# Performance work log

Hardware: AMD Instinct MI355X
Metric: run time of the kernel (lower is better)

The kernel has to match this reference:

```python
import jax, jax.numpy as jnp
import numpy as np

K = 16  # memory_topk

def signed_abs_softmax(x, axis=-1):
    # sign(x) * softmax(|x|): the module's 'signed_abs_softmax' route/edge compression
    return jnp.sign(x) * jax.nn.softmax(jnp.abs(x), axis=axis)

def unit_norm(v, eps=1e-6):
    return v / (jnp.linalg.norm(v, axis=-1, keepdims=True) + eps)

def setup_inputs() -> dict:
    key = jax.random.key(0)
    ks = jax.random.split(key, 7)
    B, T, D, S, R = 8, 2048, 512, 2048, 64
    std = 0.02
    return {
        "x": jax.random.normal(ks[0], (B, T, D), jnp.float32),
        "init_state": std * jax.random.normal(ks[1], (S,), jnp.float32),
        "init_val": std * jax.random.normal(ks[2], (S, D), jnp.float32),
        "route_a": std * jax.random.normal(ks[3], (D, R), jnp.float32),
        "route_b": std * jax.random.normal(ks[4], (R, S), jnp.float32),
        "pair_a": std * jax.random.normal(ks[5], (D, R), jnp.float32),
        "pair_b": std * jax.random.normal(ks[6], (D, R), jnp.float32),
    }

def reference(x, init_state, init_val, route_a, route_b, pair_a, pair_b):
    B, T, D = x.shape
    S = init_val.shape[0]
    b_idx = jnp.arange(B)[:, None, None]

    # --- initialize memory level (signed-softmax state, unit-norm values) ---
    state = jnp.broadcast_to(signed_abs_softmax(init_state), (B, S))
    val = jnp.broadcast_to(unit_norm(init_val), (B, S, D))

    # --- SparseTransition write: topk route tokens -> slots, scatter-add ---
    scores = jnp.einsum('btd,dr,rs->bts', x, route_a, route_b)   # [B,T,S] low-rank route
    _, idx = jax.lax.top_k(jnp.abs(scores), K)                    # [B,T,K] topk by magnitude
    g = jnp.take_along_axis(scores, idx, axis=-1)                 # signed gathered scores
    w = signed_abs_softmax(g, axis=-1)                            # route compression
    v = unit_norm(x)                                              # use_direction_only=True
    val_delta = jnp.zeros((B, S, D), x.dtype).at[b_idx, idx].add(w[..., None] * v[:, :, None, :])
    state_delta = jnp.zeros((B, S), x.dtype).at[b_idx, idx].add(jax.nn.softplus(g))
    state = signed_abs_softmax(state + state_delta, axis=-1)      # merge='add' + signed softmax state
    val = unit_norm(val + val_delta)                              # merge='add' + unit-norm values

    # --- SparsePropagation: topk pairwise edges among slots, residual mix ---
    q = jnp.einsum('bsd,dr->bsr', val, pair_a)
    kk = jnp.einsum('bsd,dr->bsr', val, pair_b)
    p = jnp.einsum('bir,bjr->bij', q, kk)                         # [B,S,S] low-rank pairwise
    _, eidx = jax.lax.top_k(jnp.abs(p), K)                        # [B,S,K] topk edges per slot
    pe = jnp.take_along_axis(p, eidx, axis=-1)
    ew = signed_abs_softmax(pe, axis=-1)                          # edge compression
    nbr = val[b_idx, eidx]                                        # [B,S,K,D] gather neighbor values
    delta = jnp.einsum('bsk,bskd->bsd', ew, nbr)
    val = unit_norm(val + delta)                                  # residual + unit-norm

    # pack (state, val) into one array: [B,S,1+D]
    return jnp.concatenate([state[..., None], val], axis=-1)
```

## Files before the change

### kernel.cpp

```cpp
#include <hip/hip_runtime.h>
#include <cmath>

namespace {
constexpr int B = 8;
constexpr int T = 2048;
constexpr int D = 512;
constexpr int S = 2048;
constexpr int R = 64;
constexpr int KTOP = 16;
constexpr int NT = 8;
constexpr int NR = 16;
constexpr int NI = 8;
constexpr int CAP = 256;
constexpr int OVFCAP = 32768;

__device__ __forceinline__ float signf(float v) {
    return (v > 0.f) ? 1.f : ((v < 0.f) ? -1.f : 0.f);
}

__device__ __forceinline__ void topk16_row(float* __restrict__ row,
                                           unsigned long long* __restrict__ cand,
                                           int lane, float& myg, int& myj) {
    const float4* p4 = (const float4*)row;
    float lmax = 0.f;
#pragma unroll
    for (int i = 0; i < 8; i++) {
        float4 v = p4[lane + 64 * i];
        lmax = fmaxf(lmax, fmaxf(fmaxf(fabsf(v.x), fabsf(v.y)),
                                 fmaxf(fabsf(v.z), fabsf(v.w))));
    }
    {
        float v = lmax;
#pragma unroll
        for (int size = 2; size <= 64; size <<= 1) {
#pragma unroll
            for (int stride = size >> 1; stride > 0; stride >>= 1) {
                float o = __shfl_xor(v, stride, 64);
                bool takeMax = ((lane & size) == 0) == ((lane & stride) == 0);
                v = takeMax ? fmaxf(v, o) : fminf(v, o);
            }
        }
        lmax = __shfl(v, 15);
    }
    float t = lmax;
    int cnt = 0;
#pragma unroll
    for (int i = 0; i < 8; i++) {
        float4 v = p4[lane + 64 * i];
        cnt += (fabsf(v.x) >= t) + (fabsf(v.y) >= t) +
               (fabsf(v.z) >= t) + (fabsf(v.w) >= t);
    }
    int off = cnt;
#pragma unroll
    for (int d = 1; d < 64; d <<= 1) {
        int o = __shfl_up(off, d, 64);
        if (lane >= d) off += o;
    }
    int total = __shfl(off, 63);
    int base = off - cnt;

    if (total <= 64) {
        int pos = base;
#pragma unroll
        for (int i = 0; i < 8; i++) {
            float4 v = p4[lane + 64 * i];
            int jb = 4 * (lane + 64 * i);
            float c[4] = {v.x, v.y, v.z, v.w};
#pragma unroll
            for (int cc = 0; cc < 4; cc++) {
                if (fabsf(c[cc]) >= t) {
                    unsigned ab = __float_as_uint(c[cc]) & 0x7fffffffu;
                    cand[pos++] = ((unsigned long long)ab << 11) |
                                  (unsigned)(2047 - (jb + cc));
                }
            }
        }
        unsigned long long key = (lane < total) ? cand[lane] : 0ull;
#pragma unroll
        for (int size = 2; size <= 64; size <<= 1) {
#pragma unroll
            for (int stride = size >> 1; stride > 0; stride >>= 1) {
                unsigned long long o = __shfl_xor((long long)key, stride, 64);
                bool takeMax = ((lane & size) == 0) == ((lane & stride) == 0);
                key = (takeMax == (key > o)) ? key : o;
            }
        }
        myg = 0.f; myj = 0;
        if (lane < KTOP) {
            myj = 2047 - (int)(key & 2047ull);
            myg = row[myj];
        }
    } else {
        myg = 0.f; myj = 0;
        for (int k = 0; k < KTOP; k++) {
            float bv = -1.f, bs = 0.f; int bj = 0;
#pragma unroll
            for (int i = 0; i < 8; i++) {
                float4 v = p4[lane + 64 * i];
                int jb = 4 * (lane + 64 * i);
                { float a = fabsf(v.x); if (a > bv) { bv = a; bs = v.x; bj = jb; } }
                { float a = fabsf(v.y); if (a > bv) { bv = a; bs = v.y; bj = jb + 1; } }
                { float a = fabsf(v.z); if (a > bv) { bv = a; bs = v.z; bj = jb + 2; } }
                { float a = fabsf(v.w); if (a > bv) { bv = a; bs = v.w; bj = jb + 3; } }
            }
#pragma unroll
            for (int off2 = 32; off2 > 0; off2 >>= 1) {
                float ov = __shfl_xor(bv, off2, 64);
                float os = __shfl_xor(bs, off2, 64);
                int   oj = __shfl_xor(bj, off2, 64);
                if (ov > bv || (ov == bv && oj < bj)) { bv = ov; bs = os; bj = oj; }
            }
            if (lane == k) { myg = bs; myj = bj; }
            if (lane == 0) row[bj] = 0.f;
        }
    }
}
}

__global__ void __launch_bounds__(512, 4) k_score(const float* __restrict__ x,
                                                  const float* __restrict__ route_a,
                                                  const float* __restrict__ route_b,
                                                  float* __restrict__ state_ws,
                                                  float* __restrict__ coef,
                                                  int* __restrict__ bincount,
                                                  int* __restrict__ binlist,
                                                  int* __restrict__ ovf_cnt,
                                                  int* __restrict__ ovf_key,
                                                  float* __restrict__ ovf_c) {
    __shared__ __align__(16) char smem[NT * S * 4];
    __shared__ __align__(16) float xr[NT][R];
    __shared__ unsigned long long cand[NT][64];
    float (*sc)[S] = (float(*)[S])smem;
    float (*xs)[D] = (float(*)[D])smem;
    float (*red4)[512] = (float(*)[512])smem;

    int tid = threadIdx.x;
    int lane = tid & 63, wv = tid >> 6;
    int blk = ((blockIdx.x & 7) << 8) | (blockIdx.x >> 3);
    int tb = blk * NT;
    int b = tb >> 11;
    int t0 = tb & (T - 1);

    {
        const float4* xg = (const float4*)(x + (size_t)tb * D);
        float4* xls = (float4*)smem;
        xls[tid] = xg[tid];
        xls[tid + 512] = xg[tid + 512];
    }
    __syncthreads();

    float xinv;
    {
        const float4* xst = (const float4*)&xs[wv][0];
        float4 x0 = xst[lane], x1 = xst[lane + 64];
        float ssx = x0.x * x0.x + x0.y * x0.y + x0.z * x0.z + x0.w * x0.w
                  + x1.x * x1.x + x1.y * x1.y + x1.z * x1.z + x1.w * x1.w;
#pragma unroll
        for (int off = 32; off > 0; off >>= 1) ssx += __shfl_xor(ssx, off, 64);
        xinv = 1.0f / (sqrtf(ssx) + 1e-6f);
    }

    {
        int r = lane;
        float acc[NT];
#pragma unroll
        for (int tt = 0; tt < NT; tt++) acc[tt] = 0.f;
        for (int d0 = wv * 64; d0 < wv * 64 + 64; d0 += 4) {
            float a0 = route_a[(size_t)(d0 + 0) * R + r];
            float a1 = route_a[(size_t)(d0 + 1) * R + r];
            float a2 = route_a[(size_t)(d0 + 2) * R + r];
            float a3 = route_a[(size_t)(d0 + 3) * R + r];
#pragma unroll
            for (int tt = 0; tt < NT; tt++) {
                float4 xv = *(const float4*)&xs[tt][d0];
                acc[tt] += xv.x * a0 + xv.y * a1 + xv.z * a2 + xv.w * a3;
            }
        }
        __syncthreads();
#pragma unroll
        for (int tt = 0; tt < NT; tt++) red4[tt][tid] = acc[tt];
        __syncthreads();
        {
            int tt2 = tid >> 6, r2 = tid & 63;
            float s = 0.f;
#pragma unroll
            for (int g = 0; g < 8; g++) s += red4[tt2][g * 64 + r2];
            xr[tt2][r2] = s;
        }
        __syncthreads();
    }

    {
        const float4* rb4 = (const float4*)route_b;
        int j4 = tid;
        float4 acc[NT];
#pragma unroll
        for (int tt = 0; tt < NT; tt++) acc[tt] = make_float4(0.f, 0.f, 0.f, 0.f);
        for (int r0 = 0; r0 < R; r0 += 4) {
            float4 xv[NT];
#pragma unroll
            for (int tt = 0; tt < NT; tt++) xv[tt] = *(const float4*)&xr[tt][r0];
#define SCORE_STEP(dr, comp)                                                   \
            {                                                                  \
                float4 bv = rb4[(size_t)(r0 + dr) * (S / 4) + j4];             \
                _Pragma("unroll")                                              \
                for (int tt = 0; tt < NT; tt++) {                              \
                    float c = xv[tt].comp;                                     \
                    acc[tt].x += c * bv.x; acc[tt].y += c * bv.y;              \
                    acc[tt].z += c * bv.z; acc[tt].w += c * bv.w;              \
                }                                                              \
            }
            SCORE_STEP(0, x) SCORE_STEP(1, y) SCORE_STEP(2, z) SCORE_STEP(3, w)
#undef SCORE_STEP
        }
#pragma unroll
        for (int tt = 0; tt < NT; tt++)
            ((float4*)&sc[tt][0])[j4] = acc[tt];
    }
    __syncthreads();

    int tt = wv;
    int tloc = t0 + tt;
    int tglob = tb + tt;

    float myg; int myj;
    topk16_row(&sc[tt][0], &cand[wv][0], lane, myg, myj);

    float m = __shfl(fabsf(myg), 0);
    float e = (lane < KTOP) ? expf(fabsf(myg) - m) : 0.f;
    float esum = e;
#pragma unroll
    for (int off = 8; off > 0; off >>= 1) esum += __shfl_xor(esum, off, 64);
    esum = __shfl(esum, 0);
    float w = signf(myg) * e / esum;
    float coefv = w * xinv;

    if (lane < KTOP) {
        float sp = (myg > 20.f) ? myg : log1pf(expf(myg));
        atomicAdd(&state_ws[(size_t)b * S + myj], sp);
        int pos = atomicAdd(&bincount[(size_t)b * S + myj], 1);
        if (pos < CAP) {
            binlist[((size_t)b * S + myj) * CAP + pos] = (tloc << 4) | lane;
            coef[(size_t)tglob * KTOP + lane] = coefv;
        } else {
            int i = atomicAdd(ovf_cnt, 1);
            if (i < OVFCAP) {
                ovf_key[i] = ((b * S + myj) << 11) | tloc;
                ovf_c[i] = coefv;
            }
        }
    }
}

__global__ void __launch_bounds__(256) k_accum(const float* __restrict__ x,
                                               const float* __restrict__ init_val,
                                               const float* __restrict__ coef,
                                               const int* __restrict__ bincount,
                                               const int* __restrict__ binlist,
                                               const int* __restrict__ ovf_cnt,
                                               const int* __restrict__ ovf_key,
                                               const float* __restrict__ ovf_c,
                                               float* __restrict__ val1) {
    int lane = threadIdx.x & 63, wv = threadIdx.x >> 6;
    int blk = ((blockIdx.x & 7) << 9) | (blockIdx.x >> 3);
    int row = blk * 4 + wv;
    int b = row >> 11;
    int s_idx = row & (S - 1);

    const float4* src = (const float4*)(init_val + (size_t)s_idx * D);
    float4 a0 = src[lane], a1 = src[lane + 64];
    {
        float ss0 = a0.x * a0.x + a0.y * a0.y + a0.z * a0.z + a0.w * a0.w
                  + a1.x * a1.x + a1.y * a1.y + a1.z * a1.z + a1.w * a1.w;
#pragma unroll
        for (int off = 32; off > 0; off >>= 1) ss0 += __shfl_xor(ss0, off, 64);
        float bsc = 1.0f / (sqrtf(ss0) + 1e-6f);
        a0.x *= bsc; a0.y *= bsc; a0.z *= bsc; a0.w *= bsc;
        a1.x *= bsc; a1.y *= bsc; a1.z *= bsc; a1.w *= bsc;
    }

    int n = bincount[row]; if (n > CAP) n = CAP;
    const int* lp = binlist + (size_t)row * CAP;
    for (int base = 0; base < n; base += 64) {
        int mm = n - base; if (mm > 64) mm = 64;
        int ent = 0; float cc = 0.f;
        if (lane < mm) {
            ent = lp[base + lane];
            cc = coef[((size_t)b * T + (ent >> 4)) * KTOP + (ent & 15)];
        }
        int e0 = __shfl(ent, 0);
        const float4* xp4 = (const float4*)(x + ((size_t)b * T + (e0 >> 4)) * D);
        float4 v0 = xp4[lane], v1 = xp4[lane + 64];
        for (int k = 0; k < mm; k++) {
            float c = __shfl(cc, k);
            float4 c0 = v0, c1 = v1;
            if (k + 1 < mm) {
                int e2 = __shfl(ent, k + 1);
                const float4* np4 = (const float4*)(x + ((size_t)b * T + (e2 >> 4)) * D);
                v0 = np4[lane]; v1 = np4[lane + 64];
            }
            a0.x += c * c0.x; a0.y += c * c0.y; a0.z += c * c0.z; a0.w += c * c0.w;
            a1.x += c * c1.x; a1.y += c * c1.y; a1.z += c * c1.z; a1.w += c * c1.w;
        }
    }

    int oc = *ovf_cnt; if (oc > OVFCAP) oc = OVFCAP;
    for (int i = 0; i < oc; i++) {
        int key = ovf_key[i];
        if ((key >> 11) == row) {
            float c = ovf_c[i];
            int tg = ((row >> 11) << 11) | (key & 2047);
            const float4* xp4 = (const float4*)(x + (size_t)tg * D);
            float4 v0 = xp4[lane], v1 = xp4[lane + 64];
            a0.x += c * v0.x; a0.y += c * v0.y; a0.z += c * v0.z; a0.w += c * v0.w;
            a1.x += c * v1.x; a1.y += c * v1.y; a1.z += c * v1.z; a1.w += c * v1.w;
        }
    }

    float ss = a0.x * a0.x + a0.y * a0.y + a0.z * a0.z + a0.w * a0.w
             + a1.x * a1.x + a1.y * a1.y + a1.z * a1.z + a1.w * a1.w;
#pragma unroll
    for (int off = 32; off > 0; off >>= 1) ss += __shfl_xor(ss, off, 64);
    float sc = 1.0f / (sqrtf(ss) + 1e-6f);
    a0.x *= sc; a0.y *= sc; a0.z *= sc; a0.w *= sc;
    a1.x *= sc; a1.y *= sc; a1.z *= sc; a1.w *= sc;
    float4* vp4 = (float4*)(val1 + (size_t)row * D);
    vp4[lane] = a0; vp4[lane + 64] = a1;
}

__global__ void __launch_bounds__(512) k_state_red(const float* __restrict__ init_state,
                                                   const float* __restrict__ state_ws,
                                                   float* base_ws,
                                                   float* sm_m, float* sm_inv) {
    __shared__ float red[16];
    __shared__ float base_lds[S];
    int tid = threadIdx.x, lane = tid & 63, wv = tid >> 6;

    float4 v = ((const float4*)init_state)[tid];
    float m = fmaxf(fmaxf(fabsf(v.x), fabsf(v.y)), fmaxf(fabsf(v.z), fabsf(v.w)));
#pragma unroll
    for (int off = 32; off > 0; off >>= 1) m = fmaxf(m, __shfl_xor(m, off, 64));
    if (lane == 0) red[wv] = m;
    __syncthreads();
    float M = red[0];
#pragma unroll
    for (int i = 1; i < 8; i++) M = fmaxf(M, red[i]);
    __syncthreads();
    float s = expf(fabsf(v.x) - M) + expf(fabsf(v.y) - M) +
              expf(fabsf(v.z) - M) + expf(fabsf(v.w) - M);
#pragma unroll
    for (int off = 32; off > 0; off >>= 1) s += __shfl_xor(s, off, 64);
    if (lane == 0) red[wv] = s;
    __syncthreads();
    float SUM = 0.f;
#pragma unroll
    for (int i = 0; i < 8; i++) SUM += red[i];
    float inv = 1.0f / SUM;
    float4 bo;
    bo.x = signf(v.x) * expf(fabsf(v.x) - M) * inv;
    bo.y = signf(v.y) * expf(fabsf(v.y) - M) * inv;
    bo.z = signf(v.z) * expf(fabsf(v.z) - M) * inv;
    bo.w = signf(v.w) * expf(fabsf(v.w) - M) * inv;
    ((float4*)base_ws)[tid] = bo;
    ((float4*)base_lds)[tid] = bo;
    __syncthreads();

    int b = wv;
    const float4* dp = (const float4*)(state_ws + (size_t)b * S);
    const float4* bp = (const float4*)base_lds;
    float4 c[8];
    float vm = 0.f;
#pragma unroll
    for (int i = 0; i < 8; i++) {
        float4 dv = dp[lane + 64 * i];
        float4 bv = bp[lane + 64 * i];
        c[i].x = bv.x + dv.x; c[i].y = bv.y + dv.y;
        c[i].z = bv.z + dv.z; c[i].w = bv.w + dv.w;
        vm = fmaxf(vm, fmaxf(fmaxf(fabsf(c[i].x), fabsf(c[i].y)),
                             fmaxf(fabsf(c[i].z), fabsf(c[i].w))));
    }
#pragma unroll
    for (int off = 32; off > 0; off >>= 1) vm = fmaxf(vm, __shfl_xor(vm, off, 64));
    float sum = 0.f;
#pragma unroll
    for (int i = 0; i < 8; i++) {
        sum += expf(fabsf(c[i].x) - vm) + expf(fabsf(c[i].y) - vm) +
               expf(fabsf(c[i].z) - vm) + expf(fabsf(c[i].w) - vm);
    }
#pragma unroll
    for (int off = 32; off > 0; off >>= 1) sum += __shfl_xor(sum, off, 64);
    if (lane == 0) { sm_m[b] = vm; sm_inv[b] = 1.0f / sum; }
}

__global__ void __launch_bounds__(256) k_qk(const float* __restrict__ val1,
                                            const float* __restrict__ pair_a,
                                            const float* __restrict__ pair_b,
                                            float* __restrict__ q,
                                            float* __restrict__ kkT) {
    __shared__ __align__(16) float vrow[NR][D];
    __shared__ float redq[256];
    __shared__ float redk[256];
    int tid = threadIdx.x;
    int blk = ((blockIdx.x & 7) << 7) | (blockIdx.x >> 3);
    int rowbase = blk * NR;
    int b = rowbase >> 11;
    int sbase = rowbase & (S - 1);
    {
        const float4* gv = (const float4*)(val1 + (size_t)rowbase * D);
        float4* lv = (float4*)&vrow[0][0];
        for (int i = tid; i < NR * D / 4; i += 256) lv[i] = gv[i];
    }
    __syncthreads();
    int r = tid & 63, grp = tid >> 6;
    float accq[NR], acck[NR];
#pragma unroll
    for (int rr = 0; rr < NR; rr++) { accq[rr] = 0.f; acck[rr] = 0.f; }
    for (int d0 = grp * 128; d0 < grp * 128 + 128; d0 += 4) {
#pragma unroll
        for (int dd = 0; dd < 4; dd++) {
            float a  = pair_a[(size_t)(d0 + dd) * R + r];
            float bb = pair_b[(size_t)(d0 + dd) * R + r];
#pragma unroll
            for (int rr = 0; rr < NR; rr++) {
                float v = vrow[rr][d0 + dd];
                accq[rr] += v * a;
                acck[rr] += v * bb;
            }
        }
    }
    for (int rr = 0; rr < NR; rr++) {
        redq[tid] = accq[rr]; redk[tid] = acck[rr];
        __syncthreads();
        if (tid < 64) {
            float qv = redq[tid] + redq[tid + 64] + redq[tid + 128] + redq[tid + 192];
            float kv = redk[tid] + redk[tid + 64] + redk[tid + 128] + redk[tid + 192];
            q[(size_t)(rowbase + rr) * R + tid] = qv;
            kkT[((size_t)b * R + tid) * S + (sbase + rr)] = kv;
        }
        __syncthreads();
    }
}

__global__ void __launch_bounds__(512) k_pscore(const float* __restrict__ q,
                                                const float* __restrict__ kkT,
                                                int* __restrict__ eidx,
                                                float* __restrict__ ew_g) {
    __shared__ __align__(16) float prow[NI][S];
    __shared__ __align__(16) float qrow[NI][R];
    __shared__ unsigned long long cand[NI][64];

    int tid = threadIdx.x;
    int lane = tid & 63, wv = tid >> 6;
    int blk = ((blockIdx.x & 7) << 8) | (blockIdx.x >> 3);
    int ibase = blk * NI;
    int b = ibase >> 11;

    {
        int rr = tid >> 6, r = tid & 63;
        qrow[rr][r] = q[(size_t)(ibase + rr) * R + r];
    }
    __syncthreads();

    {
        const float4* kk4 = (const float4*)(kkT + (size_t)b * R * S);
        int j4 = tid;
        float4 acc[NI];
#pragma unroll
        for (int rr = 0; rr < NI; rr++) acc[rr] = make_float4(0.f, 0.f, 0.f, 0.f);
        for (int r0 = 0; r0 < R; r0 += 4) {
            float4 qv[NI];
#pragma unroll
            for (int rr = 0; rr < NI; rr++) qv[rr] = *(const float4*)&qrow[rr][r0];
#define P_STEP(dr, comp)                                                       \
            {                                                                  \
                float4 kv = kk4[(size_t)(r0 + dr) * (S / 4) + j4];             \
                _Pragma("unroll")                                              \
                for (int rr = 0; rr < NI; rr++) {                              \
                    float c = qv[rr].comp;                                     \
                    acc[rr].x += c * kv.x; acc[rr].y += c * kv.y;              \
                    acc[rr].z += c * kv.z; acc[rr].w += c * kv.w;              \
                }                                                              \
            }
            P_STEP(0, x) P_STEP(1, y) P_STEP(2, z) P_STEP(3, w)
#undef P_STEP
        }
#pragma unroll
        for (int rr = 0; rr < NI; rr++)
            ((float4*)&prow[rr][0])[j4] = acc[rr];
    }
    __syncthreads();

    int row = ibase + wv;
    float myg; int myj;
    topk16_row(&prow[wv][0], &cand[wv][0], lane, myg, myj);

    float m = __shfl(fabsf(myg), 0);
    float e = (lane < KTOP) ? expf(fabsf(myg) - m) : 0.f;
    float esum = e;
#pragma unroll
    for (int off = 8; off > 0; off >>= 1) esum += __shfl_xor(esum, off, 64);
    esum = __shfl(esum, 0);
    float myw = signf(myg) * e / esum;

    if (lane < KTOP) {
        eidx[(size_t)row * KTOP + lane] = myj;
        ew_g[(size_t)row * KTOP + lane] = myw;
    }
}

__global__ void __launch_bounds__(256) k_mix(const int* __restrict__ eidx,
                                             const float* __restrict__ ew_g,
                                             const float* __restrict__ val1,
                                             const float* __restrict__ base_ws,
                                             const float* __restrict__ state_ws,
                                             const float* __restrict__ sm_m,
                                             const float* __restrict__ sm_inv,
                                             float* __restrict__ out) {
    int lane = threadIdx.x & 63, wv = threadIdx.x >> 6;
    int blk = ((blockIdx.x & 7) << 9) | (blockIdx.x >> 3);
    int row = blk * 4 + wv;
    int b = row >> 11;

    int e_i = 0; float e_w = 0.f;
    if (lane < KTOP) {
        e_i = eidx[(size_t)row * KTOP + lane];
        e_w = ew_g[(size_t)row * KTOP + lane];
    }

    const float4* self4 = (const float4*)(val1 + (size_t)row * D);
    float4 a0 = self4[lane], a1 = self4[lane + 64];
#pragma unroll
    for (int k = 0; k < KTOP; k++) {
        int j = __shfl(e_i, k);
        float w = __shfl(e_w, k);
        const float4* nb4 = (const float4*)(val1 + ((size_t)b * S + j) * D);
        float4 v0 = nb4[lane], v1 = nb4[lane + 64];
        a0.x += w * v0.x; a0.y += w * v0.y; a0.z += w * v0.z; a0.w += w * v0.w;
        a1.x += w * v1.x; a1.y += w * v1.y; a1.z += w * v1.z; a1.w += w * v1.w;
    }
    float ss = a0.x * a0.x + a0.y * a0.y + a0.z * a0.z + a0.w * a0.w
             + a1.x * a1.x + a1.y * a1.y + a1.z * a1.z + a1.w * a1.w;
#pragma unroll
    for (int off = 32; off > 0; off >>= 1) ss += __shfl_xor(ss, off, 64);
    float sc = 1.0f / (sqrtf(ss) + 1e-6f);
    float* op = out + (size_t)row * (D + 1) + 1;
    int d0 = 4 * lane;
    op[d0 + 0] = a0.x * sc; op[d0 + 1] = a0.y * sc;
    op[d0 + 2] = a0.z * sc; op[d0 + 3] = a0.w * sc;
    op[256 + d0 + 0] = a1.x * sc; op[256 + d0 + 1] = a1.y * sc;
    op[256 + d0 + 2] = a1.z * sc; op[256 + d0 + 3] = a1.w * sc;

    if (lane == 0) {
        float vv = base_ws[row & (S - 1)] + state_ws[row];
        out[(size_t)row * (D + 1)] =
            signf(vv) * expf(fabsf(vv) - sm_m[b]) * sm_inv[b];
    }
}

extern "C" void kernel_launch(void* const* d_in, const int* in_sizes, int n_in,
                              void* d_out, int out_size, void* d_ws, size_t ws_size,
                              hipStream_t stream) {
    (void)in_sizes; (void)n_in; (void)out_size; (void)ws_size;
    const float* x          = (const float*)d_in[0];
    const float* init_state = (const float*)d_in[1];
    const float* init_val   = (const float*)d_in[2];
    const float* route_a    = (const float*)d_in[3];
    const float* route_b    = (const float*)d_in[4];
    const float* pair_a     = (const float*)d_in[5];
    const float* pair_b     = (const float*)d_in[6];
    float* out = (float*)d_out;

    float* ws       = (float*)d_ws;
    float* val1     = ws;
    float* q        = val1 + (size_t)B * S * D;
    float* kkT      = q    + (size_t)B * S * R;
    float* coef     = kkT  + (size_t)B * R * S;
    int*   binlist  = (int*)(coef + (size_t)B * T * KTOP);
    float* state_ws = (float*)(binlist + (size_t)B * S * CAP);
    int*   bincount = (int*)(state_ws + (size_t)B * S);
    int*   ovf_cnt  = bincount + (size_t)B * S;
    int*   ovf_key  = ovf_cnt + 16;
    float* ovf_c    = (float*)(ovf_key + OVFCAP);
    float* base_ws  = ovf_c + OVFCAP;
    float* sm_m     = base_ws + S;
    float* sm_inv   = sm_m + B;
    int*   eidx     = binlist;
    float* ew       = (float*)(binlist + (size_t)B * S * KTOP);

    hipMemsetAsync(state_ws, 0, (size_t)(2 * B * S + 16) * sizeof(int), stream);
    hipLaunchKernelGGL(k_score, dim3(B * T / NT), dim3(512), 0, stream,
                       x, route_a, route_b, state_ws, coef, bincount, binlist,
                       ovf_cnt, ovf_key, ovf_c);
    hipLaunchKernelGGL(k_state_red, dim3(1), dim3(512), 0, stream,
                       init_state, state_ws, base_ws, sm_m, sm_inv);
    hipLaunchKernelGGL(k_accum, dim3(B * S / 4), dim3(256), 0, stream,
                       x, init_val, coef, bincount, binlist,
                       ovf_cnt, ovf_key, ovf_c, val1);
    hipLaunchKernelGGL(k_qk, dim3(B * S / NR), dim3(256), 0, stream,
                       val1, pair_a, pair_b, q, kkT);
    hipLaunchKernelGGL(k_pscore, dim3(B * S / NI), dim3(512), 0, stream,
                       q, kkT, eidx, ew);
    hipLaunchKernelGGL(k_mix, dim3(B * S / 4), dim3(256), 0, stream,
                       eidx, ew, val1, base_ws, state_ws, sm_m, sm_inv, out);
}
```

Measured before the change: 410.9 us.

## Fuse q/k projection into accumulate kernel and mix into pairwise top-k kernel

The q/k low-rank projection is folded into the value-accumulate kernel, so each block projects its four freshly normalized rows straight from shared memory instead of re-reading val1. The neighbor mix and output write are folded into the pairwise-score top-k kernel, which removes the eidx/ew round trip and two launches. The cost is less reuse of pair_a/pair_b per block (4 rows instead of 16) and a heavier pscore kernel whose occupancy and latency hiding may change.

```diff
diff --git a/kernel.cpp b/kernel.cpp
--- a/kernel.cpp
+++ b/kernel.cpp
@@ -9,7 +9,6 @@
 constexpr int R = 64;
 constexpr int KTOP = 16;
 constexpr int NT = 8;
-constexpr int NR = 16;
 constexpr int NI = 8;
 constexpr int CAP = 256;
 constexpr int OVFCAP = 32768;
@@ -252,20 +251,31 @@
     }
 }
 
-__global__ void __launch_bounds__(256) k_accum(const float* __restrict__ x,
-                                               const float* __restrict__ init_val,
-                                               const float* __restrict__ coef,
-                                               const int* __restrict__ bincount,
-                                               const int* __restrict__ binlist,
-                                               const int* __restrict__ ovf_cnt,
-                                               const int* __restrict__ ovf_key,
-                                               const float* __restrict__ ovf_c,
-                                               float* __restrict__ val1) {
-    int lane = threadIdx.x & 63, wv = threadIdx.x >> 6;
+__global__ void __launch_bounds__(256) k_accum_qk(const float* __restrict__ x,
+                                                  const float* __restrict__ init_val,
+                                                  const float* __restrict__ coef,
+                                                  const int* __restrict__ bincount,
+                                                  const int* __restrict__ binlist,
+                                                  const int* __restrict__ ovf_cnt,
+                                                  const int* __restrict__ ovf_key,
+                                                  const float* __restrict__ ovf_c,
+                                                  const float* __restrict__ pair_a,
+                                                  const float* __restrict__ pair_b,
+                                                  float* __restrict__ val1,
+                                                  float* __restrict__ q,
+                                                  float* __restrict__ kkT) {
+    __shared__ __align__(16) float vrow[4][D];
+    __shared__ float redq[4][256];
+    __shared__ float redk[4][256];
+
+    int tid = threadIdx.x;
+    int lane = tid & 63, wv = tid >> 6;
     int blk = ((blockIdx.x & 7) << 9) | (blockIdx.x >> 3);
-    int row = blk * 4 + wv;
+    int rowbase = blk * 4;
+    int row = rowbase + wv;
     int b = row >> 11;
     int s_idx = row & (S - 1);
+    int sbase = rowbase & (S - 1);
 
     const float4* src = (const float4*)(init_val + (size_t)s_idx * D);
     float4 a0 = src[lane], a1 = src[lane + 64];
@@ -326,6 +336,45 @@
     a1.x *= sc; a1.y *= sc; a1.z *= sc; a1.w *= sc;
     float4* vp4 = (float4*)(val1 + (size_t)row * D);
     vp4[lane] = a0; vp4[lane + 64] = a1;
+
+    {
+        float4* vr = (float4*)&vrow[wv][0];
+        vr[lane] = a0; vr[lane + 64] = a1;
+    }
+    __syncthreads();
+
+    int r = lane, grp = wv;
+    float accq[4], acck[4];
+#pragma unroll
+    for (int rr = 0; rr < 4; rr++) { accq[rr] = 0.f; acck[rr] = 0.f; }
+    for (int d0 = grp * 128; d0 < grp * 128 + 128; d0 += 4) {
+#pragma unroll
+        for (int dd = 0; dd < 4; dd++) {
+            float a  = pair_a[(size_t)(d0 + dd) * R + r];
+            float bb = pair_b[(size_t)(d0 + dd) * R + r];
+#pragma unroll
+            for (int rr = 0; rr < 4; rr++) {
+                float v = vrow[rr][d0 + dd];
+                accq[rr] += v * a;
+                acck[rr] += v * bb;
+            }
+        }
+    }
+#pragma unroll
+    for (int rr = 0; rr < 4; rr++) {
+        redq[rr][tid] = accq[rr];
+        redk[rr][tid] = acck[rr];
+    }
+    __syncthreads();
+    {
+        int rr = tid >> 6, r2 = tid & 63;
+        float qv = redq[rr][r2] + redq[rr][64 + r2] +
+                   redq[rr][128 + r2] + redq[rr][192 + r2];
+        float kv = redk[rr][r2] + redk[rr][64 + r2] +
+                   redk[rr][128 + r2] + redk[rr][192 + r2];
+        q[(size_t)(rowbase + rr) * R + r2] = qv;
+        kkT[((size_t)b * R + r2) * S + (sbase + rr)] = kv;
+    }
 }
 
 __global__ void __launch_bounds__(512) k_state_red(const float* __restrict__ init_state,
@@ -392,59 +441,14 @@
     if (lane == 0) { sm_m[b] = vm; sm_inv[b] = 1.0f / sum; }
 }
 
-__global__ void __launch_bounds__(256) k_qk(const float* __restrict__ val1,
-                                            const float* __restrict__ pair_a,
-                                            const float* __restrict__ pair_b,
-                                            float* __restrict__ q,
-                                            float* __restrict__ kkT) {
-    __shared__ __align__(16) float vrow[NR][D];
-    __shared__ float redq[256];
-    __shared__ float redk[256];
-    int tid = threadIdx.x;
-    int blk = ((blockIdx.x & 7) << 7) | (blockIdx.x >> 3);
-    int rowbase = blk * NR;
-    int b = rowbase >> 11;
-    int sbase = rowbase & (S - 1);
-    {
-        const float4* gv = (const float4*)(val1 + (size_t)rowbase * D);
-        float4* lv = (float4*)&vrow[0][0];
-        for (int i = tid; i < NR * D / 4; i += 256) lv[i] = gv[i];
-    }
-    __syncthreads();
-    int r = tid & 63, grp = tid >> 6;
-    float accq[NR], acck[NR];
-#pragma unroll
-    for (int rr = 0; rr < NR; rr++) { accq[rr] = 0.f; acck[rr] = 0.f; }
-    for (int d0 = grp * 128; d0 < grp * 128 + 128; d0 += 4) {
-#pragma unroll
-        for (int dd = 0; dd < 4; dd++) {
-            float a  = pair_a[(size_t)(d0 + dd) * R + r];
-            float bb = pair_b[(size_t)(d0 + dd) * R + r];
-#pragma unroll
-            for (int rr = 0; rr < NR; rr++) {
-                float v = vrow[rr][d0 + dd];
-                accq[rr] += v * a;
-                acck[rr] += v * bb;
-            }
-        }
-    }
-    for (int rr = 0; rr < NR; rr++) {
-        redq[tid] = accq[rr]; redk[tid] = acck[rr];
-        __syncthreads();
-        if (tid < 64) {
-            float qv = redq[tid] + redq[tid + 64] + redq[tid + 128] + redq[tid + 192];
-            float kv = redk[tid] + redk[tid + 64] + redk[tid + 128] + redk[tid + 192];
-            q[(size_t)(rowbase + rr) * R + tid] = qv;
-            kkT[((size_t)b * R + tid) * S + (sbase + rr)] = kv;
-        }
-        __syncthreads();
-    }
-}
-
-__global__ void __launch_bounds__(512) k_pscore(const float* __restrict__ q,
-                                                const float* __restrict__ kkT,
-                                                int* __restrict__ eidx,
-                                                float* __restrict__ ew_g) {
+__global__ void __launch_bounds__(512) k_pscore_mix(const float* __restrict__ q,
+                                                    const float* __restrict__ kkT,
+                                                    const float* __restrict__ val1,
+                                                    const float* __restrict__ base_ws,
+                                                    const float* __restrict__ state_ws,
+                                                    const float* __restrict__ sm_m,
+                                                    const float* __restrict__ sm_inv,
+                                                    float* __restrict__ out) {
     __shared__ __align__(16) float prow[NI][S];
     __shared__ __align__(16) float qrow[NI][R];
     __shared__ unsigned long long cand[NI][64];
@@ -502,37 +506,12 @@
     esum = __shfl(esum, 0);
     float myw = signf(myg) * e / esum;
 
-    if (lane < KTOP) {
-        eidx[(size_t)row * KTOP + lane] = myj;
-        ew_g[(size_t)row * KTOP + lane] = myw;
-    }
-}
-
-__global__ void __launch_bounds__(256) k_mix(const int* __restrict__ eidx,
-                                             const float* __restrict__ ew_g,
-                                             const float* __restrict__ val1,
-                                             const float* __restrict__ base_ws,
-                                             const float* __restrict__ state_ws,
-                                             const float* __restrict__ sm_m,
-                                             const float* __restrict__ sm_inv,
-                                             float* __restrict__ out) {
-    int lane = threadIdx.x & 63, wv = threadIdx.x >> 6;
-    int blk = ((blockIdx.x & 7) << 9) | (blockIdx.x >> 3);
-    int row = blk * 4 + wv;
-    int b = row >> 11;
-
-    int e_i = 0; float e_w = 0.f;
-    if (lane < KTOP) {
-        e_i = eidx[(size_t)row * KTOP + lane];
-        e_w = ew_g[(size_t)row * KTOP + lane];
-    }
-
     const float4* self4 = (const float4*)(val1 + (size_t)row * D);
     float4 a0 = self4[lane], a1 = self4[lane + 64];
 #pragma unroll
     for (int k = 0; k < KTOP; k++) {
-        int j = __shfl(e_i, k);
-        float w = __shfl(e_w, k);
+        int j = __shfl(myj, k);
+        float w = __shfl(myw, k);
         const float4* nb4 = (const float4*)(val1 + ((size_t)b * S + j) * D);
         float4 v0 = nb4[lane], v1 = nb4[lane + 64];
         a0.x += w * v0.x; a0.y += w * v0.y; a0.z += w * v0.z; a0.w += w * v0.w;
@@ -542,13 +521,13 @@
              + a1.x * a1.x + a1.y * a1.y + a1.z * a1.z + a1.w * a1.w;
 #pragma unroll
     for (int off = 32; off > 0; off >>= 1) ss += __shfl_xor(ss, off, 64);
-    float sc = 1.0f / (sqrtf(ss) + 1e-6f);
+    float scale = 1.0f / (sqrtf(ss) + 1e-6f);
     float* op = out + (size_t)row * (D + 1) + 1;
     int d0 = 4 * lane;
-    op[d0 + 0] = a0.x * sc; op[d0 + 1] = a0.y * sc;
-    op[d0 + 2] = a0.z * sc; op[d0 + 3] = a0.w * sc;
-    op[256 + d0 + 0] = a1.x * sc; op[256 + d0 + 1] = a1.y * sc;
-    op[256 + d0 + 2] = a1.z * sc; op[256 + d0 + 3] = a1.w * sc;
+    op[d0 + 0] = a0.x * scale; op[d0 + 1] = a0.y * scale;
+    op[d0 + 2] = a0.z * scale; op[d0 + 3] = a0.w * scale;
+    op[256 + d0 + 0] = a1.x * scale; op[256 + d0 + 1] = a1.y * scale;
+    op[256 + d0 + 2] = a1.z * scale; op[256 + d0 + 3] = a1.w * scale;
 
     if (lane == 0) {
         float vv = base_ws[row & (S - 1)] + state_ws[row];
@@ -584,8 +563,6 @@
     float* base_ws  = ovf_c + OVFCAP;
     float* sm_m     = base_ws + S;
     float* sm_inv   = sm_m + B;
-    int*   eidx     = binlist;
-    float* ew       = (float*)(binlist + (size_t)B * S * KTOP);
 
     hipMemsetAsync(state_ws, 0, (size_t)(2 * B * S + 16) * sizeof(int), stream);
     hipLaunchKernelGGL(k_score, dim3(B * T / NT), dim3(512), 0, stream,
@@ -593,13 +570,9 @@
                        ovf_cnt, ovf_key, ovf_c);
     hipLaunchKernelGGL(k_state_red, dim3(1), dim3(512), 0, stream,
                        init_state, state_ws, base_ws, sm_m, sm_inv);
-    hipLaunchKernelGGL(k_accum, dim3(B * S / 4), dim3(256), 0, stream,
+    hipLaunchKernelGGL(k_accum_qk, dim3(B * S / 4), dim3(256), 0, stream,
                        x, init_val, coef, bincount, binlist,
-                       ovf_cnt, ovf_key, ovf_c, val1);
-    hipLaunchKernelGGL(k_qk, dim3(B * S / NR), dim3(256), 0, stream,
-                       val1, pair_a, pair_b, q, kkT);
-    hipLaunchKernelGGL(k_pscore, dim3(B * S / NI), dim3(512), 0, stream,
-                       q, kkT, eidx, ew);
-    hipLaunchKernelGGL(k_mix, dim3(B * S / 4), dim3(256), 0, stream,
-                       eidx, ew, val1, base_ws, state_ws, sm_m, sm_inv, out);
-}
+                       ovf_cnt, ovf_key, ovf_c, pair_a, pair_b, val1, q, kkT);
+    hipLaunchKernelGGL(k_pscore_mix, dim3(B * S / NI), dim3(512), 0, stream,
+                       q, kkT, val1, base_ws, state_ws, sm_m, sm_inv, out);
+}
```

Result: faster. 392.8 us (-4.4%).
